# Performance work log

Hardware: AMD Instinct MI355X
Metric: run time of the kernel (lower is better)

Reference implementation:

```python
import jax, jax.numpy as jnp
import numpy as np

N_NODES = 10000
N_EDGES = 320000
N_GRAPHS = 64
D_IN = 256
D_HID = 256
D_OUT = 16


def sage_conv(x, edge_index, w_l, b_l, w_r):
    # PyG SAGEConv: out = lin_l(mean_{j in N(i)} x_j) + lin_r(x_i)
    src, dst = edge_index[0], edge_index[1]
    msg = x[src]                                   # [E, d] gather
    summed = jax.ops.segment_sum(msg, dst, num_segments=x.shape[0])
    ones = jnp.ones((edge_index.shape[1],), dtype=x.dtype)
    cnt = jax.ops.segment_sum(ones, dst, num_segments=x.shape[0])
    aggr = summed / jnp.maximum(cnt, 1.0)[:, None]  # mean aggregation
    return aggr @ w_l.T + b_l + x @ w_r.T


def setup_inputs() -> dict:
    key = jax.random.key(0)
    ks = jax.random.split(key, 12)

    def glorot(k, shape):
        lim = float(np.sqrt(6.0 / (shape[0] + shape[1])))
        return jax.random.uniform(k, shape, jnp.float32, -lim, lim)

    x = jax.random.normal(ks[0], (N_NODES, D_IN), jnp.float32)
    edge_index = jax.random.randint(ks[1], (2, N_EDGES), 0, N_NODES, jnp.int64)
    batch = jnp.sort(jax.random.randint(ks[2], (N_NODES,), 0, N_GRAPHS, jnp.int64))

    return {
        "x": x,
        "edge_index": edge_index,
        "batch": batch,
        "w1_l": glorot(ks[3], (D_HID, D_IN)),
        "b1_l": jnp.zeros((D_HID,), jnp.float32),
        "w1_r": glorot(ks[4], (D_HID, D_IN)),
        "w2_l": glorot(ks[5], (D_HID, D_HID)),
        "b2_l": jnp.zeros((D_HID,), jnp.float32),
        "w2_r": glorot(ks[6], (D_HID, D_HID)),
        "w_cls": glorot(ks[7], (D_OUT, D_HID)),
        "b_cls": jnp.zeros((D_OUT,), jnp.float32),
    }


def reference(x, edge_index, batch, w1_l, b1_l, w1_r, w2_l, b2_l, w2_r, w_cls, b_cls):
    h = jax.nn.relu(sage_conv(x, edge_index, w1_l, b1_l, w1_r))
    h = jax.nn.relu(sage_conv(h, edge_index, w2_l, b2_l, w2_r))
    pooled = jax.ops.segment_sum(h, batch, num_segments=N_GRAPHS)  # global_add_pool
    return jax.nn.sigmoid(pooled @ w_cls.T + b_cls)
```

## Files before the change

kernel.cpp:

```cpp
#include <hip/hip_runtime.h>
#include <hip/hip_fp16.h>
#include <math.h>

#define NN 10000
#define NE 320000
#define NG 64
#define DD 256
#define DOUT 16
#define SLOT 96

typedef __attribute__((ext_vector_type(8))) _Float16 f16x8;
typedef __attribute__((ext_vector_type(4))) float f32x4;

#define OFF_CNT   0u
#define OFF_CSR   40064u
#define OFF_XH    3880064u
#define OFF_AGGR  9000064u
#define OFF_H1    14120064u
#define OFF_H2    19240064u
#define OFF_WH    24360064u
#define OFF_POOL  24884352u

__device__ __forceinline__ void gload16(const void* g, void* l) {
  __builtin_amdgcn_global_load_lds(
      (const __attribute__((address_space(1))) void*)g,
      (__attribute__((address_space(3))) void*)l, 16, 0, 0);
}

__global__ __launch_bounds__(256) void init_kernel(int* __restrict__ cnt,
                                                   float* __restrict__ pooled) {
  int i = blockIdx.x * 256 + threadIdx.x;
  if (i < NN) cnt[i] = 0;
  if (i < NG * DD) pooled[i] = 0.f;
}

#define NFB 1250
#define NXG (NN * DD / 8)
#define NWG 8192
#define NCB ((NXG + 4 * NWG + 255) / 256)
__global__ __launch_bounds__(256) void prep_kernel(
    const int* __restrict__ ei, int* __restrict__ cnt, int* __restrict__ csr,
    const float* __restrict__ x, const float* __restrict__ w1l,
    const float* __restrict__ w1r, const float* __restrict__ w2l,
    const float* __restrict__ w2r, _Float16* __restrict__ xh,
    _Float16* __restrict__ wh) {
  if (blockIdx.x < NFB) {
    int e = blockIdx.x * 256 + threadIdx.x;
    int s = ei[e];
    int d = ei[NE + e];
    int p = atomicAdd(&cnt[d], 1);
    if (p < SLOT) csr[d * SLOT + p] = s;
    return;
  }
  int i = (blockIdx.x - NFB) * 256 + threadIdx.x;
  const float* src;
  _Float16* dst;
  if (i < NXG) {
    src = x + i * 8;
    dst = xh + i * 8;
  } else if (i < NXG + 4 * NWG) {
    int j = i - NXG;
    int w = j >> 13, k = j & (NWG - 1);
    src = ((w == 0) ? w1l : (w == 1) ? w1r : (w == 2) ? w2l : w2r) + k * 8;
    dst = wh + w * 65536 + k * 8;
  } else {
    return;
  }
  const float4* sp = (const float4*)src;
  float4 a = sp[0], b = sp[1];
  f16x8 r;
  r[0] = (_Float16)a.x; r[1] = (_Float16)a.y; r[2] = (_Float16)a.z; r[3] = (_Float16)a.w;
  r[4] = (_Float16)b.x; r[5] = (_Float16)b.y; r[6] = (_Float16)b.z; r[7] = (_Float16)b.w;
  *(f16x8*)dst = r;
}

__global__ __launch_bounds__(256) void aggregate_f16_kernel(
    const _Float16* __restrict__ xin, const int* __restrict__ cnt,
    const int* __restrict__ csr, _Float16* __restrict__ out) {
  const int wave = threadIdx.x >> 6, lane = threadIdx.x & 63;
  const int node = blockIdx.x * 4 + wave;
  if (node >= NN) return;
  const int deg = cnt[node];
  const int n = min(deg, SLOT);
  const int base = node * SLOT;
  const int h = lane >> 5;
  const int cb = (lane & 31) * 8;
  float a[8] = {0.f, 0.f, 0.f, 0.f, 0.f, 0.f, 0.f, 0.f};
  int i = h;
  for (; i + 14 < n; i += 16) {
    f16x8 v[8];
#pragma unroll
    for (int u = 0; u < 8; ++u) {
      int s = csr[base + i + 2 * u];
      v[u] = *(const f16x8*)&xin[s * DD + cb];
    }
#pragma unroll
    for (int j = 0; j < 8; ++j)
      a[j] += (((float)v[0][j] + (float)v[1][j]) + ((float)v[2][j] + (float)v[3][j])) +
              (((float)v[4][j] + (float)v[5][j]) + ((float)v[6][j] + (float)v[7][j]));
  }
  for (; i < n; i += 2) {
    int s = csr[base + i];
    f16x8 v = *(const f16x8*)&xin[s * DD + cb];
#pragma unroll
    for (int j = 0; j < 8; ++j) a[j] += (float)v[j];
  }
#pragma unroll
  for (int j = 0; j < 8; ++j) a[j] += __shfl_xor(a[j], 32);
  if (lane < 32) {
    float inv = 1.0f / fmaxf((float)deg, 1.0f);
    f16x8 r;
#pragma unroll
    for (int j = 0; j < 8; ++j) r[j] = (_Float16)(a[j] * inv);
    *(f16x8*)&out[node * DD + cb] = r;
  }
}

__global__ __launch_bounds__(256) void gemm_mfma_kernel(
    const _Float16* __restrict__ A1, const _Float16* __restrict__ A2,
    const _Float16* __restrict__ W1, const _Float16* __restrict__ W2,
    const float* __restrict__ bias, _Float16* __restrict__ out) {
  __shared__ _Float16 As[2][128 * 64];
  __shared__ _Float16 Bs[2][64 * 64];
  const int id = blockIdx.x;
  const int xcd = id & 7;
  const int q = id >> 3;
  const int cblk = q & 3;
  const int rblk = (q >> 2) * 8 + xcd;
  const int row0 = rblk * 128, col0 = cblk * 64;
  if (row0 >= NN) return;

  const int t = threadIdx.x;
  const int lane = t & 63;
  const int wid = t >> 6;
  const int wr = wid >> 1, wc = wid & 1;
  const int fr = lane & 15;
  const int fg = lane >> 4;
  const int srl = lane >> 3;
  const int cj = lane & 7;

  f32x4 acc[4][2];
#pragma unroll
  for (int m = 0; m < 4; ++m)
#pragma unroll
    for (int n = 0; n < 2; ++n) {
      acc[m][n][0] = 0.f; acc[m][n][1] = 0.f;
      acc[m][n][2] = 0.f; acc[m][n][3] = 0.f;
    }

#define STAGE(B, S)                                                           \
  {                                                                           \
    const _Float16* Ap = ((S) < 4) ? A1 : A2;                                 \
    const _Float16* Wp = ((S) < 4) ? W1 : W2;                                 \
    const int k0 = ((S) & 3) * 64;                                            \
    _Pragma("unroll") for (int j = 0; j < 4; ++j) {                           \
      int row = (wid * 4 + j) * 8 + srl;                          \
      int gr = row0 + row; if (gr >= NN) gr = NN - 1;                         \
      int gc = cj ^ (row & 7);                                                \
      gload16(Ap + (size_t)gr * DD + k0 + gc * 8, &As[B][(wid * 4 + j) * 512]);\
    }                                                                         \
    _Pragma("unroll") for (int j = 0; j < 2; ++j) {                           \
      int row = (wid * 2 + j) * 8 + srl;                           \
      int gc = cj ^ (row & 7);                                                \
      gload16(Wp + (size_t)(col0 + row) * DD + k0 + gc * 8,                   \
              &Bs[B][(wid * 2 + j) * 512]);                                   \
    }                                                                         \
  }

  STAGE(0, 0);
  __syncthreads();

#pragma unroll
  for (int s = 0; s < 8; ++s) {
    const int b = s & 1;
    if (s < 7) STAGE(1 - b, s + 1);
#pragma unroll
    for (int kk = 0; kk < 2; ++kk) {
      f16x8 af[4], bf[2];
#pragma unroll
      for (int m = 0; m < 4; ++m) {
        int row = wr * 64 + m * 16 + fr;
        int ch = (kk * 4 + fg) ^ (row & 7);
        af[m] = *(const f16x8*)&As[b][row * 64 + ch * 8];
      }
#pragma unroll
      for (int n = 0; n < 2; ++n) {
        int row = wc * 32 + n * 16 + fr;
        int ch = (kk * 4 + fg) ^ (row & 7);
        bf[n] = *(const f16x8*)&Bs[b][row * 64 + ch * 8];
      }
#pragma unroll
      for (int m = 0; m < 4; ++m)
#pragma unroll
        for (int n = 0; n < 2; ++n)
          acc[m][n] = __builtin_amdgcn_mfma_f32_16x16x32_f16(af[m], bf[n], acc[m][n], 0, 0, 0);
    }
    __syncthreads();
  }
#undef STAGE

  const int orow = row0 + wr * 64 + (lane >> 4) * 4;
  const int ocol = col0 + wc * 32 + fr;
#pragma unroll
  for (int m = 0; m < 4; ++m)
#pragma unroll
    for (int n = 0; n < 2; ++n) {
      int col = ocol + n * 16;
      float bv = bias[col];
#pragma unroll
      for (int j = 0; j < 4; ++j) {
        int row = orow + m * 16 + j;
        if (row < NN) {
          float v = acc[m][n][j] + bv;
          out[row * DD + col] = (_Float16)fmaxf(v, 0.f);
        }
      }
    }
}

__global__ __launch_bounds__(256) void pool_chunk_kernel(const _Float16* __restrict__ h2,
                                                         const int* __restrict__ batch,
                                                         float* __restrict__ pooled) {
  const int c = threadIdx.x;
  const int n0 = blockIdx.x * 16;
  float acc = 0.f;
  int g = batch[n0];
  for (int i = n0; i < n0 + 16; ++i) {
    int gi = batch[i];
    if (gi != g) {
      atomicAdd(&pooled[g * DD + c], acc);
      acc = 0.f;
      g = gi;
    }
    acc += (float)h2[i * DD + c];
  }
  atomicAdd(&pooled[g * DD + c], acc);
}

__global__ __launch_bounds__(256) void cls_kernel(const float* __restrict__ pooled,
                                                  const float* __restrict__ wc,
                                                  const float* __restrict__ bc,
                                                  float* __restrict__ out) {
  int t = blockIdx.x * 256 + threadIdx.x;
  if (t >= NG * DOUT) return;
  int g = t >> 4, j = t & 15;
  float s = bc[j];
  for (int k = 0; k < DD; k += 4) {
    float4 p = *(const float4*)&pooled[g * DD + k];
    float4 w = *(const float4*)&wc[j * DD + k];
    s += p.x * w.x + p.y * w.y + p.z * w.z + p.w * w.w;
  }
  out[t] = 1.0f / (1.0f + expf(-s));
}

extern "C" void kernel_launch(void* const* d_in, const int* in_sizes, int n_in,
                              void* d_out, int out_size, void* d_ws, size_t ws_size,
                              hipStream_t stream) {
  const float* x     = (const float*)d_in[0];
  const int*   ei    = (const int*)d_in[1];
  const int*   batch = (const int*)d_in[2];
  const float* w1_l  = (const float*)d_in[3];
  const float* b1_l  = (const float*)d_in[4];
  const float* w1_r  = (const float*)d_in[5];
  const float* w2_l  = (const float*)d_in[6];
  const float* b2_l  = (const float*)d_in[7];
  const float* w2_r  = (const float*)d_in[8];
  const float* w_cls = (const float*)d_in[9];
  const float* b_cls = (const float*)d_in[10];
  float* out = (float*)d_out;

  char* ws = (char*)d_ws;
  int*       cnt    = (int*)(ws + OFF_CNT);
  int*       csr    = (int*)(ws + OFF_CSR);
  _Float16*  xh     = (_Float16*)(ws + OFF_XH);
  _Float16*  aggr   = (_Float16*)(ws + OFF_AGGR);
  _Float16*  h1     = (_Float16*)(ws + OFF_H1);
  _Float16*  h2     = (_Float16*)(ws + OFF_H2);
  _Float16*  wh     = (_Float16*)(ws + OFF_WH);
  float*     pooled = (float*)(ws + OFF_POOL);

  init_kernel<<<64, 256, 0, stream>>>(cnt, pooled);

  prep_kernel<<<NFB + NCB, 256, 0, stream>>>(ei, cnt, csr, x, w1_l, w1_r,
                                             w2_l, w2_r, xh, wh);

  const int agrid = (NN + 3) / 4;

  aggregate_f16_kernel<<<agrid, 256, 0, stream>>>(xh, cnt, csr, aggr);
  gemm_mfma_kernel<<<320, 256, 0, stream>>>(aggr, xh, wh, wh + 65536, b1_l, h1);

  aggregate_f16_kernel<<<agrid, 256, 0, stream>>>(h1, cnt, csr, aggr);
  gemm_mfma_kernel<<<320, 256, 0, stream>>>(aggr, h1, wh + 2 * 65536, wh + 3 * 65536, b2_l, h2);

  pool_chunk_kernel<<<(NN + 15) / 16, 256, 0, stream>>>(h2, batch, pooled);
  cls_kernel<<<4, 256, 0, stream>>>(pooled, w_cls, b_cls, out);
}
```

Before: 111.9 us.

## Shrink GEMM row tile to 64 with XCD-contiguous mapping; store CSR as u16

New measurement: 105.8 us (median of 2 runs). 5.4% less time.

```diff
diff --git a/kernel.cpp b/kernel.cpp
--- a/kernel.cpp
+++ b/kernel.cpp
@@ -14,12 +14,12 @@
 
 #define OFF_CNT   0u
 #define OFF_CSR   40064u
-#define OFF_XH    3880064u
-#define OFF_AGGR  9000064u
-#define OFF_H1    14120064u
-#define OFF_H2    19240064u
-#define OFF_WH    24360064u
-#define OFF_POOL  24884352u
+#define OFF_XH    1960064u
+#define OFF_AGGR  7080064u
+#define OFF_H1    12200064u
+#define OFF_H2    17320064u
+#define OFF_WH    22440064u
+#define OFF_POOL  22964352u
 
 __device__ __forceinline__ void gload16(const void* g, void* l) {
   __builtin_amdgcn_global_load_lds(
@@ -39,7 +39,8 @@
 #define NWG 8192
 #define NCB ((NXG + 4 * NWG + 255) / 256)
 __global__ __launch_bounds__(256) void prep_kernel(
-    const int* __restrict__ ei, int* __restrict__ cnt, int* __restrict__ csr,
+    const int* __restrict__ ei, int* __restrict__ cnt,
+    unsigned short* __restrict__ csr,
     const float* __restrict__ x, const float* __restrict__ w1l,
     const float* __restrict__ w1r, const float* __restrict__ w2l,
     const float* __restrict__ w2r, _Float16* __restrict__ xh,
@@ -49,7 +50,7 @@
     int s = ei[e];
     int d = ei[NE + e];
     int p = atomicAdd(&cnt[d], 1);
-    if (p < SLOT) csr[d * SLOT + p] = s;
+    if (p < SLOT) csr[d * SLOT + p] = (unsigned short)s;
     return;
   }
   int i = (blockIdx.x - NFB) * 256 + threadIdx.x;
@@ -76,7 +77,7 @@
 
 __global__ __launch_bounds__(256) void aggregate_f16_kernel(
     const _Float16* __restrict__ xin, const int* __restrict__ cnt,
-    const int* __restrict__ csr, _Float16* __restrict__ out) {
+    const unsigned short* __restrict__ csr, _Float16* __restrict__ out) {
   const int wave = threadIdx.x >> 6, lane = threadIdx.x & 63;
   const int node = blockIdx.x * 4 + wave;
   if (node >= NN) return;
@@ -120,15 +121,14 @@
     const _Float16* __restrict__ A1, const _Float16* __restrict__ A2,
     const _Float16* __restrict__ W1, const _Float16* __restrict__ W2,
     const float* __restrict__ bias, _Float16* __restrict__ out) {
-  __shared__ _Float16 As[2][128 * 64];
+  __shared__ _Float16 As[2][64 * 64];
   __shared__ _Float16 Bs[2][64 * 64];
-  const int id = blockIdx.x;
-  const int xcd = id & 7;
-  const int q = id >> 3;
-  const int cblk = q & 3;
-  const int rblk = (q >> 2) * 8 + xcd;
-  const int row0 = rblk * 128, col0 = cblk * 64;
-  if (row0 >= NN) return;
+  const int xcd = blockIdx.x & 7;
+  const int q = blockIdx.x >> 3;
+  const int T = xcd * 79 + q;
+  if (T >= 628) return;
+  const int rblk = T >> 2, cblk = T & 3;
+  const int row0 = rblk * 64, col0 = cblk * 64;
 
   const int t = threadIdx.x;
   const int lane = t & 63;
@@ -139,9 +139,9 @@
   const int srl = lane >> 3;
   const int cj = lane & 7;
 
-  f32x4 acc[4][2];
-#pragma unroll
-  for (int m = 0; m < 4; ++m)
+  f32x4 acc[2][2];
+#pragma unroll
+  for (int m = 0; m < 2; ++m)
 #pragma unroll
     for (int n = 0; n < 2; ++n) {
       acc[m][n][0] = 0.f; acc[m][n][1] = 0.f;
@@ -153,17 +153,14 @@
     const _Float16* Ap = ((S) < 4) ? A1 : A2;                                 \
     const _Float16* Wp = ((S) < 4) ? W1 : W2;                                 \
     const int k0 = ((S) & 3) * 64;                                            \
-    _Pragma("unroll") for (int j = 0; j < 4; ++j) {                           \
-      int row = (wid * 4 + j) * 8 + srl;                          \
+    const int gc = cj ^ srl;                                \
+    _Pragma("unroll") for (int j = 0; j < 2; ++j) {                           \
+      int row = j * 32 + wid * 8 + srl;                                       \
       int gr = row0 + row; if (gr >= NN) gr = NN - 1;                         \
-      int gc = cj ^ (row & 7);                                                \
-      gload16(Ap + (size_t)gr * DD + k0 + gc * 8, &As[B][(wid * 4 + j) * 512]);\
-    }                                                                         \
-    _Pragma("unroll") for (int j = 0; j < 2; ++j) {                           \
-      int row = (wid * 2 + j) * 8 + srl;                           \
-      int gc = cj ^ (row & 7);                                                \
+      gload16(Ap + (size_t)gr * DD + k0 + gc * 8,                             \
+              &As[B][(j * 32 + wid * 8) * 64]);                               \
       gload16(Wp + (size_t)(col0 + row) * DD + k0 + gc * 8,                   \
-              &Bs[B][(wid * 2 + j) * 512]);                                   \
+              &Bs[B][(j * 32 + wid * 8) * 64]);                               \
     }                                                                         \
   }
 
@@ -176,10 +173,10 @@
     if (s < 7) STAGE(1 - b, s + 1);
 #pragma unroll
     for (int kk = 0; kk < 2; ++kk) {
-      f16x8 af[4], bf[2];
-#pragma unroll
-      for (int m = 0; m < 4; ++m) {
-        int row = wr * 64 + m * 16 + fr;
+      f16x8 af[2], bf[2];
+#pragma unroll
+      for (int m = 0; m < 2; ++m) {
+        int row = wr * 32 + m * 16 + fr;
         int ch = (kk * 4 + fg) ^ (row & 7);
         af[m] = *(const f16x8*)&As[b][row * 64 + ch * 8];
       }
@@ -190,7 +187,7 @@
         bf[n] = *(const f16x8*)&Bs[b][row * 64 + ch * 8];
       }
 #pragma unroll
-      for (int m = 0; m < 4; ++m)
+      for (int m = 0; m < 2; ++m)
 #pragma unroll
         for (int n = 0; n < 2; ++n)
           acc[m][n] = __builtin_amdgcn_mfma_f32_16x16x32_f16(af[m], bf[n], acc[m][n], 0, 0, 0);
@@ -199,10 +196,10 @@
   }
 #undef STAGE
 
-  const int orow = row0 + wr * 64 + (lane >> 4) * 4;
+  const int orow = row0 + wr * 32 + (lane >> 4) * 4;
   const int ocol = col0 + wc * 32 + fr;
 #pragma unroll
-  for (int m = 0; m < 4; ++m)
+  for (int m = 0; m < 2; ++m)
 #pragma unroll
     for (int n = 0; n < 2; ++n) {
       int col = ocol + n * 16;
@@ -270,14 +267,14 @@
   float* out = (float*)d_out;
 
   char* ws = (char*)d_ws;
-  int*       cnt    = (int*)(ws + OFF_CNT);
-  int*       csr    = (int*)(ws + OFF_CSR);
-  _Float16*  xh     = (_Float16*)(ws + OFF_XH);
-  _Float16*  aggr   = (_Float16*)(ws + OFF_AGGR);
-  _Float16*  h1     = (_Float16*)(ws + OFF_H1);
-  _Float16*  h2     = (_Float16*)(ws + OFF_H2);
-  _Float16*  wh     = (_Float16*)(ws + OFF_WH);
-  float*     pooled = (float*)(ws + OFF_POOL);
+  int*            cnt    = (int*)(ws + OFF_CNT);
+  unsigned short* csr    = (unsigned short*)(ws + OFF_CSR);
+  _Float16*       xh     = (_Float16*)(ws + OFF_XH);
+  _Float16*       aggr   = (_Float16*)(ws + OFF_AGGR);
+  _Float16*       h1     = (_Float16*)(ws + OFF_H1);
+  _Float16*       h2     = (_Float16*)(ws + OFF_H2);
+  _Float16*       wh     = (_Float16*)(ws + OFF_WH);
+  float*          pooled = (float*)(ws + OFF_POOL);
 
   init_kernel<<<64, 256, 0, stream>>>(cnt, pooled);
 
@@ -287,10 +284,10 @@
   const int agrid = (NN + 3) / 4;
 
   aggregate_f16_kernel<<<agrid, 256, 0, stream>>>(xh, cnt, csr, aggr);
-  gemm_mfma_kernel<<<320, 256, 0, stream>>>(aggr, xh, wh, wh + 65536, b1_l, h1);
+  gemm_mfma_kernel<<<632, 256, 0, stream>>>(aggr, xh, wh, wh + 65536, b1_l, h1);
 
   aggregate_f16_kernel<<<agrid, 256, 0, stream>>>(h1, cnt, csr, aggr);
-  gemm_mfma_kernel<<<320, 256, 0, stream>>>(aggr, h1, wh + 2 * 65536, wh + 3 * 65536, b2_l, h2);
+  gemm_mfma_kernel<<<632, 256, 0, stream>>>(aggr, h1, wh + 2 * 65536, wh + 3 * 65536, b2_l, h2);
 
   pool_chunk_kernel<<<(NN + 15) / 16, 256, 0, stream>>>(h2, batch, pooled);
   cls_kernel<<<4, 256, 0, stream>>>(pooled, w_cls, b_cls, out);
```
